# Optimization experiments

Measured on AMD Instinct MI355X. Metric: run time of the kernel, lower is better.

## Reference

```python
import jax, jax.numpy as jnp
import numpy as np

N, T = 4096, 1024
COND, PRED, PERIOD = 896, 56, 7


def setup_inputs() -> dict:
    key = jax.random.key(0)
    k1, k2 = jax.random.split(key)
    query = jax.random.normal(k1, (N, T), dtype=jnp.float32)
    # learned per-location params: [init_level, level_sm_logit, init_trend,
    #  trend_sm_logit, season_sm, period seasonality logits]
    params = 0.1 * jax.random.normal(k2, (N, 5 + PERIOD), dtype=jnp.float32)
    return {"query": query, "params": params}


def _forward(query, params):
    init_level = params[:, 0]                       # [N]
    level_sm = jax.nn.sigmoid(params[:, 1])         # [N]
    init_trend = params[:, 2]                       # [N]
    trend_sm = jax.nn.sigmoid(params[:, 3])         # [N]
    season_sm = params[:, 4]                        # NOTE: no sigmoid, matches original code
    init_seas = jax.nn.sigmoid(params[:, -PERIOD:])  # [N, PERIOD]

    def step(carry, y):
        prev_level, prev_trend, buf = carry          # buf: rolling window of last PERIOD seasonalities
        s_t = buf[:, 0]                              # seasonalities[t]
        pred = prev_level + prev_trend
        level = level_sm * y + (1.0 - level_sm) * pred
        diff = jnp.abs(level - prev_level)
        trend = trend_sm * (level - prev_level) + (1.0 - trend_sm) * prev_trend
        new_seas = season_sm * (y - pred) + (1.0 - season_sm) * s_t
        buf = jnp.concatenate([buf[:, 1:], new_seas[:, None]], axis=1)
        return (level, trend, buf), (level, trend, new_seas, diff)

    carry0 = (init_level, init_trend, init_seas)
    _, (levels, trends, new_seas_seq, diffs) = jax.lax.scan(step, carry0, query.T)
    levels = levels.T            # [N, T]
    trends = trends.T            # [N, T]
    new_seas_seq = new_seas_seq.T  # [N, T], == seasonalities[:, PERIOD:]
    level_diffs = diffs.T.mean(axis=1)  # [N]

    # full seasonality sequence: PERIOD initial values followed by T computed ones
    seas_full = jnp.concatenate([init_seas, new_seas_seq], axis=1)  # [N, PERIOD+T]

    sm = query - levels - new_seas_seq  # [N, T]

    horizon = jnp.arange(1, PRED + 1, dtype=levels.dtype)  # [PRED]
    last_levels = levels[:, COND - 1:, None]   # [N, W, 1], W = T-COND+1
    last_trends = trends[:, COND - 1:, None]
    pr = last_levels + last_trends * horizon   # [N, W, PRED]

    # cyclic seasonality forecast per window
    season_index = jnp.tile(jnp.arange(PERIOD), (PRED + PERIOD - 1) // PERIOD)[:PRED]
    starts = jnp.arange(COND, T + 1)           # [W]
    idx = starts[:, None] + season_index[None, :]  # [W, PRED]
    pr = pr + seas_full[:, idx]                # [N, W, PRED]

    return sm, pr, level_diffs


def reference(query, params):
    return _forward(query, params)
```

## Files before the change

### kernel.cpp

```cpp
#include <hip/hip_runtime.h>
#include <cmath>

#define NROWS 4096
#define TLEN  1024
#define RPB   8
#define LT0   895
#define ST0   889
#define LTN   129
#define STN   135
#define PRV4R 1806
#define PRV4B (RPB * PRV4R)

typedef float f32x4 __attribute__((ext_vector_type(4)));

__device__ __forceinline__ float sigmoidf_(float x) {
    return 1.0f / (1.0f + expf(-x));
}

__device__ __forceinline__ float f4c(const float4& v, int k) {
    switch (k & 3) { case 0: return v.x; case 1: return v.y; case 2: return v.z; default: return v.w; }
}

__device__ __forceinline__ void nt_store4(float4* p, const float4& v) {
    f32x4 t; t.x = v.x; t.y = v.y; t.z = v.z; t.w = v.w;
    __builtin_nontemporal_store(t, reinterpret_cast<f32x4*>(p));
}

#define PR_EMIT(qv_)                                                          \
    {                                                                         \
        const int q_   = (qv_);                                               \
        const int row_ = q_ / PRV4R;                                          \
        const int rem_ = q_ - row_ * PRV4R;                                   \
        const int s_   = rem_ / 14;                                           \
        const int h4_  = rem_ - s_ * 14;                                      \
        const float L_ = Ltl[row_ * 132 + s_];                                \
        const float T_ = Ttl[row_ * 132 + s_];                                \
        const float* stp_ = &Stl[row_ * 136 + s_];                            \
        const int hb_ = h4_ * 4;                                              \
        int m0_ = hb_ % 7;                                                    \
        int m1_ = m0_ + 1; if (m1_ >= 7) m1_ -= 7;                            \
        int m2_ = m1_ + 1; if (m2_ >= 7) m2_ -= 7;                            \
        int m3_ = m2_ + 1; if (m3_ >= 7) m3_ -= 7;                            \
        const float hbf_ = (float)hb_;                                        \
        float4 o_;                                                            \
        o_.x = fmaf(T_, hbf_ + 1.0f, L_) + stp_[m0_];                         \
        o_.y = fmaf(T_, hbf_ + 2.0f, L_) + stp_[m1_];                         \
        o_.z = fmaf(T_, hbf_ + 3.0f, L_) + stp_[m2_];                         \
        o_.w = fmaf(T_, hbf_ + 4.0f, L_) + stp_[m3_];                         \
        nt_store4(&prb[q_], o_);                                              \
    }

__global__ __launch_bounds__(512, 2)
void es_fused(const float* __restrict__ query,
              const float* __restrict__ params,
              float* __restrict__ sm,
              float* __restrict__ diffs,
              float4* __restrict__ pr4)
{
    __shared__ float4 ystage[RPB * 256];
    __shared__ float lds_P[RPB * 65];
    __shared__ float lds_start[RPB * 65];
    __shared__ float lds_q[RPB * 225];
    __shared__ float lds_dsum[RPB * 33];
    __shared__ float lds_par[RPB * 16];
    __shared__ float Ltl[RPB * 132];
    __shared__ float Ttl[RPB * 132];
    __shared__ float Stl[RPB * 136];

    const int tid = threadIdx.x;
    const int base = blockIdx.x * RPB;
    const int r = (tid >> 5) & 7;
    const int k = tid & 31;
    const int n = base + r;

    {
        const float4* qb = reinterpret_cast<const float4*>(query + (size_t)base * TLEN);
        #pragma unroll
        for (int i = 0; i < 4; ++i) {
            const int w = i * 512 + tid;
            ystage[(w & ~7) | ((w ^ (w >> 3)) & 7)] = qb[w];
        }
    }

    float a = 0.f, b = 0.f, c = 0.f, ia = 0.f, ib = 0.f, ic = 0.f;
    if (tid < 256) {
        const float* pp = params + (size_t)n * 12;
        a  = sigmoidf_(pp[1]);
        b  = sigmoidf_(pp[3]);
        c  = pp[4];
        ia = 1.0f - a; ib = 1.0f - b; ic = 1.0f - c;
        if (k == 0) {
            float* par = &lds_par[r * 16];
            par[0] = pp[0];
            par[1] = pp[2];
            par[2] = ia;
            par[3] = -(a * b);
            par[4] = ib + b * ia;
            par[5] = ic;
            #pragma unroll
            for (int l = 0; l < 7; ++l) par[6 + l] = sigmoidf_(pp[5 + l]);
        }
    }
    __syncthreads();

    float4 yv[8];
    float e[32];
    float st0 = 0.f, st1 = 0.f;

    if (tid < 256) {
        const int ksw = k & 7;
        #pragma unroll
        for (int i = 0; i < 8; ++i)
            yv[i] = ystage[r * 256 + ((k * 8 + i) ^ ksw)];

        float L = 0.0f, B = 0.0f;
        #pragma unroll
        for (int j = 0; j < 32; ++j) {
            const float yy = f4c(yv[j >> 2], j);
            const float pred  = L + B;
            const float level = fmaf(a, yy, ia * pred);
            const float trend = fmaf(b, level - L, ib * B);
            L = level; B = trend;
        }
        lds_P[r * 65 + 2 * k]     = L;
        lds_P[r * 65 + 2 * k + 1] = B;
    }
    __syncthreads();

    if (tid < 8) {
        const float* par = &lds_par[tid * 16];
        float m00 = par[2], m01 = par[2], m10 = par[3], m11 = par[4];
        #pragma unroll
        for (int s = 0; s < 5; ++s) {
            const float t00 = m00 * m00 + m01 * m10;
            const float t01 = m00 * m01 + m01 * m11;
            const float t10 = m10 * m00 + m11 * m10;
            const float t11 = m10 * m01 + m11 * m11;
            m00 = t00; m01 = t01; m10 = t10; m11 = t11;
        }
        float P0[32], P1[32];
        #pragma unroll
        for (int kk = 0; kk < 32; ++kk) {
            P0[kk] = lds_P[tid * 65 + 2 * kk];
            P1[kk] = lds_P[tid * 65 + 2 * kk + 1];
        }
        float s0 = par[0], s1 = par[1];
        #pragma unroll
        for (int kk = 0; kk < 32; ++kk) {
            lds_start[tid * 65 + 2 * kk]     = s0;
            lds_start[tid * 65 + 2 * kk + 1] = s1;
            const float t0 = m00 * s0 + m01 * s1 + P0[kk];
            const float t1 = m10 * s0 + m11 * s1 + P1[kk];
            s0 = t0; s1 = t1;
        }
    }
    __syncthreads();

    if (tid < 256) {
        st0 = lds_start[r * 65 + 2 * k];
        st1 = lds_start[r * 65 + 2 * k + 1];
        float L = st0, B = st1, dsum = 0.0f;
        float q[7] = {0,0,0,0,0,0,0};
        #pragma unroll
        for (int j = 0; j < 32; ++j) {
            const float yy = f4c(yv[j >> 2], j);
            const float pred  = L + B;
            const float level = fmaf(a, yy, ia * pred);
            const float d     = level - L;
            dsum += fabsf(d);
            const float trend = fmaf(b, d, ib * B);
            const float ee    = yy - pred;
            e[j] = ee;
            q[j % 7] = fmaf(ic, q[j % 7], c * ee);
            L = level; B = trend;
        }
        const int kp = (4 * k) % 7;
        #pragma unroll
        for (int l = 0; l < 7; ++l) {
            int g = kp + l; if (g >= 7) g -= 7;
            lds_q[r * 225 + k * 7 + g] = q[l];
        }
        lds_dsum[r * 33 + k] = dsum;

        if (k >= 27) {
            float prevL = st0, Bv = st1;
            #pragma unroll
            for (int j = 0; j < 32; ++j) {
                const float level = f4c(yv[j >> 2], j) - ia * e[j];
                const float trend = fmaf(b, level - prevL, ib * Bv);
                const int tg = k * 32 + j;
                if (tg >= LT0) {
                    Ltl[r * 132 + tg - LT0] = level;
                    Ttl[r * 132 + tg - LT0] = trend;
                }
                prevL = level; Bv = trend;
            }
        }
    }
    __syncthreads();

    if (tid < 56) {
        const int rr = tid / 7, p = tid % 7;
        const float icc = lds_par[rr * 16 + 5];
        const float ic2 = icc * icc;
        const float ic4 = ic2 * ic2;
        const float ic5 = ic4 * icc;
        float v = lds_par[rr * 16 + 6 + p];
        float qq[32];
        #pragma unroll
        for (int kk = 0; kk < 32; ++kk) qq[kk] = lds_q[rr * 225 + kk * 7 + p];
        int l = p;
        #pragma unroll
        for (int kk = 0; kk < 32; ++kk) {
            const float m = (l < 4) ? ic5 : ic4;
            const float nv = fmaf(m, v, qq[kk]);
            lds_q[rr * 225 + kk * 7 + p] = v;
            v = nv;
            l += 3; if (l >= 7) l -= 7;
        }
    } else if (tid < 64) {
        const int rr = tid - 56;
        float s = 0.0f;
        #pragma unroll
        for (int kk = 0; kk < 32; ++kk) s += lds_dsum[rr * 33 + kk];
        diffs[blockIdx.x * RPB + rr] = s * (1.0f / 1024.0f);
    }
    __syncthreads();

    if (tid < 256) {
        float sg[7];
        const int kp = (4 * k) % 7;
        #pragma unroll
        for (int l = 0; l < 7; ++l) {
            int g = kp + l; if (g >= 7) g -= 7;
            sg[l] = lds_q[r * 225 + k * 7 + g];
        }
        const int ksw = k & 7;
        float4 ov;
        #pragma unroll
        for (int j = 0; j < 32; ++j) {
            const float sn = fmaf(ic, sg[j % 7], c * e[j]);
            sg[j % 7] = sn;
            const float smv = ia * e[j] - sn;
            e[j] = sn;
            switch (j & 3) { case 0: ov.x = smv; break; case 1: ov.y = smv; break;
                             case 2: ov.z = smv; break; default: ov.w = smv; }
            if ((j & 3) == 3)
                ystage[r * 256 + ((k * 8 + (j >> 2)) ^ ksw)] = ov;
        }
        if (k >= 27) {
            #pragma unroll
            for (int j = 0; j < 32; ++j) {
                const int tg = k * 32 + j;
                if (tg >= ST0) Stl[r * 136 + tg - ST0] = e[j];
            }
        }
    }
    __syncthreads();

    {
        float4* smb = reinterpret_cast<float4*>(sm + (size_t)base * TLEN);
        #pragma unroll
        for (int i = 0; i < 4; ++i) {
            const int w = i * 512 + tid;
            const float4 v = ystage[(w & ~7) | ((w ^ (w >> 3)) & 7)];
            nt_store4(&smb[w], v);
        }
    }

    {
        float4* prb = pr4 + (size_t)blockIdx.x * PRV4B;
        #pragma unroll 4
        for (int i = 0; i < 28; ++i) {
            PR_EMIT(i * 512 + tid);
        }
        const int q = 28 * 512 + tid;
        if (q < PRV4B) {
            PR_EMIT(q);
        }
    }
}

extern "C" void kernel_launch(void* const* d_in, const int* in_sizes, int n_in,
                              void* d_out, int out_size, void* d_ws, size_t ws_size,
                              hipStream_t stream) {
    const float* query  = (const float*)d_in[0];
    const float* params = (const float*)d_in[1];

    float* out   = (float*)d_out;
    float* sm    = out;
    float* pr    = out + (size_t)NROWS * TLEN;
    float* diffs = pr  + (size_t)NROWS * 129 * 56;

    hipLaunchKernelGGL(es_fused, dim3(NROWS / RPB), dim3(512), 0, stream,
                       query, params, sm, diffs, (float4*)pr);
}
```

Baseline: 37.86 us.

## Halve rows per block, spill error sequence to LDS, drop nontemporal stores

Reduces rows per block from 8 to 4, doubling the grid, and raises the launch-bounds occupancy hint from 2 to 6 blocks. The per-thread e[32] register array is moved into the LDS staging buffer, and the tail level/trend recompute now runs the recurrence directly instead of using e. Nontemporal stores are replaced with ordinary stores. The goal is fewer registers and more resident waves to hide memory latency, at the cost of extra LDS traffic and an added barrier.

After: 49.29 us. 1.3x slower.

```diff
diff --git a/kernel.cpp b/kernel.cpp
--- a/kernel.cpp
+++ b/kernel.cpp
@@ -3,7 +3,7 @@
 
 #define NROWS 4096
 #define TLEN  1024
-#define RPB   8
+#define RPB   4
 #define LT0   895
 #define ST0   889
 #define LTN   129
@@ -11,19 +11,12 @@
 #define PRV4R 1806
 #define PRV4B (RPB * PRV4R)
 
-typedef float f32x4 __attribute__((ext_vector_type(4)));
-
 __device__ __forceinline__ float sigmoidf_(float x) {
     return 1.0f / (1.0f + expf(-x));
 }
 
 __device__ __forceinline__ float f4c(const float4& v, int k) {
     switch (k & 3) { case 0: return v.x; case 1: return v.y; case 2: return v.z; default: return v.w; }
-}
-
-__device__ __forceinline__ void nt_store4(float4* p, const float4& v) {
-    f32x4 t; t.x = v.x; t.y = v.y; t.z = v.z; t.w = v.w;
-    __builtin_nontemporal_store(t, reinterpret_cast<f32x4*>(p));
 }
 
 #define PR_EMIT(qv_)                                                          \
@@ -47,10 +40,10 @@
         o_.y = fmaf(T_, hbf_ + 2.0f, L_) + stp_[m1_];                         \
         o_.z = fmaf(T_, hbf_ + 3.0f, L_) + stp_[m2_];                         \
         o_.w = fmaf(T_, hbf_ + 4.0f, L_) + stp_[m3_];                         \
-        nt_store4(&prb[q_], o_);                                              \
-    }
-
-__global__ __launch_bounds__(512, 2)
+        prb[q_] = o_;                                                         \
+    }
+
+__global__ __launch_bounds__(512, 6)
 void es_fused(const float* __restrict__ query,
               const float* __restrict__ params,
               float* __restrict__ sm,
@@ -67,23 +60,25 @@
     __shared__ float Ttl[RPB * 132];
     __shared__ float Stl[RPB * 136];
 
+    float* ef = reinterpret_cast<float*>(ystage);
+
     const int tid = threadIdx.x;
     const int base = blockIdx.x * RPB;
-    const int r = (tid >> 5) & 7;
+    const int r = (tid >> 5) & 3;
     const int k = tid & 31;
     const int n = base + r;
 
     {
         const float4* qb = reinterpret_cast<const float4*>(query + (size_t)base * TLEN);
         #pragma unroll
-        for (int i = 0; i < 4; ++i) {
+        for (int i = 0; i < 2; ++i) {
             const int w = i * 512 + tid;
             ystage[(w & ~7) | ((w ^ (w >> 3)) & 7)] = qb[w];
         }
     }
 
     float a = 0.f, b = 0.f, c = 0.f, ia = 0.f, ib = 0.f, ic = 0.f;
-    if (tid < 256) {
+    if (tid < 128) {
         const float* pp = params + (size_t)n * 12;
         a  = sigmoidf_(pp[1]);
         b  = sigmoidf_(pp[3]);
@@ -104,10 +99,9 @@
     __syncthreads();
 
     float4 yv[8];
-    float e[32];
     float st0 = 0.f, st1 = 0.f;
 
-    if (tid < 256) {
+    if (tid < 128) {
         const int ksw = k & 7;
         #pragma unroll
         for (int i = 0; i < 8; ++i)
@@ -127,7 +121,7 @@
     }
     __syncthreads();
 
-    if (tid < 8) {
+    if (tid < 4) {
         const float* par = &lds_par[tid * 16];
         float m00 = par[2], m01 = par[2], m10 = par[3], m11 = par[4];
         #pragma unroll
@@ -156,7 +150,7 @@
     }
     __syncthreads();
 
-    if (tid < 256) {
+    if (tid < 128) {
         st0 = lds_start[r * 65 + 2 * k];
         st1 = lds_start[r * 65 + 2 * k + 1];
         float L = st0, B = st1, dsum = 0.0f;
@@ -170,7 +164,7 @@
             dsum += fabsf(d);
             const float trend = fmaf(b, d, ib * B);
             const float ee    = yy - pred;
-            e[j] = ee;
+            ef[r * 1024 + j * 32 + k] = ee;
             q[j % 7] = fmaf(ic, q[j % 7], c * ee);
             L = level; B = trend;
         }
@@ -186,7 +180,9 @@
             float prevL = st0, Bv = st1;
             #pragma unroll
             for (int j = 0; j < 32; ++j) {
-                const float level = f4c(yv[j >> 2], j) - ia * e[j];
+                const float yy = f4c(yv[j >> 2], j);
+                const float pred  = prevL + Bv;
+                const float level = fmaf(a, yy, ia * pred);
                 const float trend = fmaf(b, level - prevL, ib * Bv);
                 const int tg = k * 32 + j;
                 if (tg >= LT0) {
@@ -199,7 +195,7 @@
     }
     __syncthreads();
 
-    if (tid < 56) {
+    if (tid < 28) {
         const int rr = tid / 7, p = tid % 7;
         const float icc = lds_par[rr * 16 + 5];
         const float ic2 = icc * icc;
@@ -218,8 +214,8 @@
             v = nv;
             l += 3; if (l >= 7) l -= 7;
         }
-    } else if (tid < 64) {
-        const int rr = tid - 56;
+    } else if (tid < 32) {
+        const int rr = tid - 28;
         float s = 0.0f;
         #pragma unroll
         for (int kk = 0; kk < 32; ++kk) s += lds_dsum[rr * 33 + kk];
@@ -227,7 +223,8 @@
     }
     __syncthreads();
 
-    if (tid < 256) {
+    float4 ov[8];
+    if (tid < 128) {
         float sg[7];
         const int kp = (4 * k) % 7;
         #pragma unroll
@@ -235,48 +232,47 @@
             int g = kp + l; if (g >= 7) g -= 7;
             sg[l] = lds_q[r * 225 + k * 7 + g];
         }
+        #pragma unroll
+        for (int j = 0; j < 32; ++j) {
+            const float ee = ef[r * 1024 + j * 32 + k];
+            const float sn = fmaf(ic, sg[j % 7], c * ee);
+            sg[j % 7] = sn;
+            const float smv = ia * ee - sn;
+            switch (j & 3) { case 0: ov[j >> 2].x = smv; break;
+                             case 1: ov[j >> 2].y = smv; break;
+                             case 2: ov[j >> 2].z = smv; break;
+                             default: ov[j >> 2].w = smv; }
+            const int tg = k * 32 + j;
+            if (tg >= ST0) Stl[r * 136 + tg - ST0] = sn;
+        }
+    }
+    __syncthreads();
+
+    if (tid < 128) {
         const int ksw = k & 7;
-        float4 ov;
-        #pragma unroll
-        for (int j = 0; j < 32; ++j) {
-            const float sn = fmaf(ic, sg[j % 7], c * e[j]);
-            sg[j % 7] = sn;
-            const float smv = ia * e[j] - sn;
-            e[j] = sn;
-            switch (j & 3) { case 0: ov.x = smv; break; case 1: ov.y = smv; break;
-                             case 2: ov.z = smv; break; default: ov.w = smv; }
-            if ((j & 3) == 3)
-                ystage[r * 256 + ((k * 8 + (j >> 2)) ^ ksw)] = ov;
-        }
-        if (k >= 27) {
-            #pragma unroll
-            for (int j = 0; j < 32; ++j) {
-                const int tg = k * 32 + j;
-                if (tg >= ST0) Stl[r * 136 + tg - ST0] = e[j];
-            }
-        }
+        #pragma unroll
+        for (int i = 0; i < 8; ++i)
+            ystage[r * 256 + ((k * 8 + i) ^ ksw)] = ov[i];
     }
     __syncthreads();
 
     {
         float4* smb = reinterpret_cast<float4*>(sm + (size_t)base * TLEN);
         #pragma unroll
-        for (int i = 0; i < 4; ++i) {
+        for (int i = 0; i < 2; ++i) {
             const int w = i * 512 + tid;
-            const float4 v = ystage[(w & ~7) | ((w ^ (w >> 3)) & 7)];
-            nt_store4(&smb[w], v);
+            smb[w] = ystage[(w & ~7) | ((w ^ (w >> 3)) & 7)];
         }
     }
 
     {
         float4* prb = pr4 + (size_t)blockIdx.x * PRV4B;
         #pragma unroll 4
-        for (int i = 0; i < 28; ++i) {
+        for (int i = 0; i < 14; ++i) {
             PR_EMIT(i * 512 + tid);
         }
-        const int q = 28 * 512 + tid;
-        if (q < PRV4B) {
-            PR_EMIT(q);
+        if (tid < PRV4B - 14 * 512) {
+            PR_EMIT(14 * 512 + tid);
         }
     }
 }
```
